# Kernel tuning notes

Hardware: AMD Instinct MI355X
Metric: run time of the kernel (lower is better)

## Reference

```python
import jax, jax.numpy as jnp
import numpy as np

N_HEAD = 16
HEAD_DIM = 128  # n_embd // n_head
EPS = 1e-6
ROPE_BASE = 10000.0


def rmsnorm(x, w):
    rms = jnp.mean(x * x, axis=-1, keepdims=True)
    return w * (x * jax.lax.rsqrt(rms + EPS))


def rope_cache(T, head_dim):
    half = head_dim // 2
    inv_freq = 1.0 / (ROPE_BASE ** (jnp.arange(half, dtype=jnp.float32) / half))
    pos = jnp.arange(T, dtype=jnp.float32)
    freqs = pos[:, None] * inv_freq[None, :]  # [T, half]
    return jnp.cos(freqs), jnp.sin(freqs)


def apply_rope(x, cos, sin):
    # x: [B, H, T, D]; cos/sin: [T, D/2]
    half = x.shape[-1] // 2
    x1, x2 = x[..., :half], x[..., half:]
    return jnp.concatenate([x1 * cos - x2 * sin, x1 * sin + x2 * cos], axis=-1)


def setup_inputs() -> dict:
    key = jax.random.key(0)
    ks = jax.random.split(key, 8)
    B, T, C, Hid = 2, 2048, 2048, 5632
    s = 0.02
    return {
        "x": jax.random.normal(ks[0], (B, T, C), dtype=jnp.float32),
        "w_norm1": jnp.ones((C,), dtype=jnp.float32),
        "w_qkv": jax.random.normal(ks[1], (C, 3 * C), dtype=jnp.float32) * s,
        "w_proj": jax.random.normal(ks[2], (C, C), dtype=jnp.float32) * s,
        "w_norm2": jnp.ones((C,), dtype=jnp.float32),
        "w1": jax.random.normal(ks[3], (C, Hid), dtype=jnp.float32) * s,
        "w2": jax.random.normal(ks[4], (C, Hid), dtype=jnp.float32) * s,
        "w3": jax.random.normal(ks[5], (Hid, C), dtype=jnp.float32) * s,
    }


def reference(x, w_norm1, w_qkv, w_proj, w_norm2, w1, w2, w3):
    B, T, C = x.shape
    H, D = N_HEAD, HEAD_DIM

    # ---- attention branch ----
    h = rmsnorm(x, w_norm1)
    qkv = h @ w_qkv  # [B, T, 3C]
    q, k, v = jnp.split(qkv, 3, axis=-1)
    q = q.reshape(B, T, H, D).transpose(0, 2, 1, 3)  # [B,H,T,D]
    k = k.reshape(B, T, H, D).transpose(0, 2, 1, 3)
    v = v.reshape(B, T, H, D).transpose(0, 2, 1, 3)

    cos, sin = rope_cache(T, D)
    q = apply_rope(q, cos, sin)
    k = apply_rope(k, cos, sin)

    att = jnp.einsum('bhqd,bhkd->bhqk', q, k) / np.sqrt(D).astype(np.float32)
    causal = jnp.tril(jnp.ones((T, T), dtype=bool))
    att = jnp.where(causal, att, -jnp.inf)
    att = jax.nn.softmax(att, axis=-1)
    out = jnp.einsum('bhqk,bhkd->bhqd', att, v)
    out = out.transpose(0, 2, 1, 3).reshape(B, T, C)
    x = x + out @ w_proj

    # ---- SwiGLU MLP branch ----
    h2 = rmsnorm(x, w_norm2)
    x = x + (jax.nn.silu(h2 @ w1) * (h2 @ w2)) @ w3
    return x
```

## Files before the change

### kernel.cpp

```cpp
#include <hip/hip_runtime.h>

typedef short s16x8 __attribute__((ext_vector_type(8)));
typedef unsigned short u16;
typedef u16 u16x8 __attribute__((ext_vector_type(8)));
typedef u16 u16x4 __attribute__((ext_vector_type(4)));
typedef float f32x4 __attribute__((ext_vector_type(4)));

#define DEVINL __device__ __forceinline__

DEVINL u16 f2bf(float f) {
    unsigned u = __float_as_uint(f);
    u += 0x7FFFu + ((u >> 16) & 1u);
    return (u16)(u >> 16);
}
DEVINL float bf2f(u16 h) { return __uint_as_float((unsigned)h << 16); }

DEVINL void gl2lds16(const void* g, void* l) {
    __builtin_amdgcn_global_load_lds((const __attribute__((address_space(1))) void*)g,
                                     (__attribute__((address_space(3))) void*)l, 16, 0, 0);
}

DEVINL void tcast_tile(const float* __restrict__ src, u16* __restrict__ dst,
                       const int K, const int N, const int kx, const int ny,
                       const int tid, float (*tile)[33])
{
    const long k0 = (long)kx * 32;
    const long n0 = (long)ny * 32;
    const int r = tid >> 3, c4 = (tid & 7) * 4;
    float4 v = *(const float4*)&src[(k0 + r) * N + n0 + c4];
    tile[r][c4] = v.x; tile[r][c4 + 1] = v.y; tile[r][c4 + 2] = v.z; tile[r][c4 + 3] = v.w;
    __syncthreads();
    u16x4 ov;
    ov[0] = f2bf(tile[c4][r]);     ov[1] = f2bf(tile[c4 + 1][r]);
    ov[2] = f2bf(tile[c4 + 2][r]); ov[3] = f2bf(tile[c4 + 3][r]);
    *(u16x4*)&dst[(n0 + r) * K + k0 + c4] = ov;
}

__global__ __launch_bounds__(256) void tcast4(
    const float* __restrict__ s0, const float* __restrict__ s1,
    const float* __restrict__ s2, const float* __restrict__ s3,
    u16* __restrict__ d0, u16* __restrict__ d1,
    u16* __restrict__ d2, u16* __restrict__ d3)
{
    __shared__ float tile[32][33];
    int t = blockIdx.x;
    const float* src; u16* dst; int N;
    if (t < 12288)      {             src = s0; dst = d0; N = 6144; }
    else if (t < 16384) { t -= 12288; src = s1; dst = d1; N = 2048; }
    else if (t < 27648) { t -= 16384; src = s2; dst = d2; N = 5632; }
    else                { t -= 27648; src = s3; dst = d3; N = 5632; }
    tcast_tile(src, dst, 2048, N, t & 63, t >> 6, threadIdx.x, tile);
}

__global__ __launch_bounds__(256) void tcast(
    const float* __restrict__ src, u16* __restrict__ dst, const int K, const int N)
{
    __shared__ float tile[32][33];
    tcast_tile(src, dst, K, N, blockIdx.x, blockIdx.y, threadIdx.x, tile);
}

__global__ __launch_bounds__(256) void rmsnorm_cast(
    const float* __restrict__ x, const float* __restrict__ wn, u16* __restrict__ out)
{
    const int C = 2048;
    const long row = blockIdx.x;
    const int tid = threadIdx.x;
    const float4* xr = (const float4*)(x + row * C);
    float4 a = xr[tid * 2], b = xr[tid * 2 + 1];
    float ss = a.x*a.x + a.y*a.y + a.z*a.z + a.w*a.w
             + b.x*b.x + b.y*b.y + b.z*b.z + b.w*b.w;
#pragma unroll
    for (int m = 1; m < 64; m <<= 1) ss += __shfl_xor(ss, m);
    __shared__ float red[4];
    if ((tid & 63) == 0) red[tid >> 6] = ss;
    __syncthreads();
    float scale = rsqrtf((red[0] + red[1] + red[2] + red[3]) * (1.f / 2048.f) + 1e-6f);
    const float4* wr = (const float4*)wn;
    float4 wa = wr[tid * 2], wb = wr[tid * 2 + 1];
    u16x8 o;
    o[0] = f2bf(a.x * scale * wa.x); o[1] = f2bf(a.y * scale * wa.y);
    o[2] = f2bf(a.z * scale * wa.z); o[3] = f2bf(a.w * scale * wa.w);
    o[4] = f2bf(b.x * scale * wb.x); o[5] = f2bf(b.y * scale * wb.y);
    o[6] = f2bf(b.z * scale * wb.z); o[7] = f2bf(b.w * scale * wb.w);
    *(u16x8*)&out[row * C + tid * 8] = o;
}

template <int MODE>
__global__ __launch_bounds__(256, 2) void gemm128(
    const u16* __restrict__ A, const u16* __restrict__ Bt,
    const int N, const int K,
    float* __restrict__ outF, u16* __restrict__ outB,
    const float* __restrict__ resid)
{
    __shared__ u16 As[128 * 64];
    __shared__ u16 Bs[128 * 64];
    const int tid = threadIdx.x;
    const int lane = tid & 63;
    const int w = tid >> 6;
    const int wm = w >> 1, wn = w & 1;
    const int quad = lane >> 4, l16 = lane & 15;
    const long m0 = (long)blockIdx.x * 128;
    const long n0 = (long)blockIdx.y * 128;

    const u16* ga[4]; const u16* gb[4]; char* la[4]; char* lb[4];
#pragma unroll
    for (int rr = 0; rr < 4; ++rr) {
        int idx = rr * 256 + tid;
        int r = idx >> 3, j = idx & 7;
        int c = (j ^ (r & 7)) * 8;
        ga[rr] = A + (m0 + r) * K + c;
        gb[rr] = Bt + (n0 + r) * K + c;
        la[rr] = (char*)As + idx * 16;
        lb[rr] = (char*)Bs + idx * 16;
    }

    f32x4 acc[4][4] = {};

    for (int k0 = 0; k0 < K; k0 += 64) {
#pragma unroll
        for (int rr = 0; rr < 4; ++rr) {
            gl2lds16(ga[rr] + k0, la[rr]);
            gl2lds16(gb[rr] + k0, lb[rr]);
        }
        __syncthreads();
#pragma unroll
        for (int ks = 0; ks < 2; ++ks) {
            s16x8 af[4], bfv[4];
#pragma unroll
            for (int mt = 0; mt < 4; ++mt)
                af[mt] = *(const s16x8*)&As[(wm * 64 + mt * 16 + l16) * 64 +
                                            ((ks * 4 + quad) ^ (l16 & 7)) * 8];
#pragma unroll
            for (int nt = 0; nt < 4; ++nt)
                bfv[nt] = *(const s16x8*)&Bs[(wn * 64 + nt * 16 + l16) * 64 +
                                             ((ks * 4 + quad) ^ (l16 & 7)) * 8];
#pragma unroll
            for (int mt = 0; mt < 4; ++mt)
#pragma unroll
                for (int nt = 0; nt < 4; ++nt)
                    acc[mt][nt] = __builtin_amdgcn_mfma_f32_16x16x32_bf16(af[mt], bfv[nt], acc[mt][nt], 0, 0, 0);
        }
        __syncthreads();
    }

#pragma unroll
    for (int mt = 0; mt < 4; ++mt)
#pragma unroll
        for (int reg = 0; reg < 4; ++reg) {
            long row = m0 + wm * 64 + mt * 16 + quad * 4 + reg;
#pragma unroll
            for (int nt = 0; nt < 4; ++nt) {
                long col = n0 + wn * 64 + nt * 16 + l16;
                float v = acc[mt][nt][reg];
                if (MODE == 0) {
                    outB[row * N + col] = f2bf(v);
                } else {
                    outF[row * N + col] = resid[row * N + col] + v;
                }
            }
        }
}

__global__ __launch_bounds__(256, 2) void gemm_ffn(
    const u16* __restrict__ A, const u16* __restrict__ B1t, const u16* __restrict__ B2t,
    const int N, const int K, u16* __restrict__ outB)
{
    __shared__ u16 As[128 * 64];
    __shared__ u16 B1s[128 * 64];
    __shared__ u16 B2s[128 * 64];
    const int tid = threadIdx.x;
    const int lane = tid & 63;
    const int w = tid >> 6;
    const int wm = w >> 1, wn = w & 1;
    const int quad = lane >> 4, l16 = lane & 15;
    const long m0 = (long)blockIdx.x * 128;
    const long n0 = (long)blockIdx.y * 128;

    const u16* ga[4]; const u16* gb1[4]; const u16* gb2[4];
    char* la[4]; char* lb1[4]; char* lb2[4];
#pragma unroll
    for (int rr = 0; rr < 4; ++rr) {
        int idx = rr * 256 + tid;
        int r = idx >> 3, j = idx & 7;
        int c = (j ^ (r & 7)) * 8;
        ga[rr]  = A + (m0 + r) * K + c;
        gb1[rr] = B1t + (n0 + r) * K + c;
        gb2[rr] = B2t + (n0 + r) * K + c;
        la[rr]  = (char*)As + idx * 16;
        lb1[rr] = (char*)B1s + idx * 16;
        lb2[rr] = (char*)B2s + idx * 16;
    }

    f32x4 acc1[4][4] = {};
    f32x4 acc2[4][4] = {};

    for (int k0 = 0; k0 < K; k0 += 64) {
#pragma unroll
        for (int rr = 0; rr < 4; ++rr) {
            gl2lds16(ga[rr] + k0, la[rr]);
            gl2lds16(gb1[rr] + k0, lb1[rr]);
            gl2lds16(gb2[rr] + k0, lb2[rr]);
        }
        __syncthreads();
#pragma unroll
        for (int ks = 0; ks < 2; ++ks) {
            s16x8 af[4], b1f[4], b2f[4];
#pragma unroll
            for (int mt = 0; mt < 4; ++mt)
                af[mt] = *(const s16x8*)&As[(wm * 64 + mt * 16 + l16) * 64 +
                                            ((ks * 4 + quad) ^ (l16 & 7)) * 8];
#pragma unroll
            for (int nt = 0; nt < 4; ++nt) {
                b1f[nt] = *(const s16x8*)&B1s[(wn * 64 + nt * 16 + l16) * 64 +
                                              ((ks * 4 + quad) ^ (l16 & 7)) * 8];
                b2f[nt] = *(const s16x8*)&B2s[(wn * 64 + nt * 16 + l16) * 64 +
                                              ((ks * 4 + quad) ^ (l16 & 7)) * 8];
            }
#pragma unroll
            for (int mt = 0; mt < 4; ++mt)
#pragma unroll
                for (int nt = 0; nt < 4; ++nt) {
                    acc1[mt][nt] = __builtin_amdgcn_mfma_f32_16x16x32_bf16(af[mt], b1f[nt], acc1[mt][nt], 0, 0, 0);
                    acc2[mt][nt] = __builtin_amdgcn_mfma_f32_16x16x32_bf16(af[mt], b2f[nt], acc2[mt][nt], 0, 0, 0);
                }
        }
        __syncthreads();
    }

#pragma unroll
    for (int mt = 0; mt < 4; ++mt)
#pragma unroll
        for (int reg = 0; reg < 4; ++reg) {
            long row = m0 + wm * 64 + mt * 16 + quad * 4 + reg;
#pragma unroll
            for (int nt = 0; nt < 4; ++nt) {
                long col = n0 + wn * 64 + nt * 16 + l16;
                float g = acc1[mt][nt][reg];
                float s = g / (1.f + __expf(-g));
                outB[row * N + col] = f2bf(s * acc2[mt][nt][reg]);
            }
        }
}

__global__ __launch_bounds__(256) void rope_qk(
    const u16* __restrict__ qkv, u16* __restrict__ qT, u16* __restrict__ kT)
{
    const int row = blockIdx.x;
    const int t = row & 2047, b = row >> 11;
    const int tid = threadIdx.x;
    __shared__ u16 buf[4096];
    const u16* src = qkv + (long)row * 6144;
    u16x8 aa = *(const u16x8*)&src[tid * 8];
    u16x8 kk = *(const u16x8*)&src[2048 + tid * 8];
    *(u16x8*)&buf[tid * 8] = aa;
    *(u16x8*)&buf[2048 + tid * 8] = kk;
    __syncthreads();
    const int c = tid * 8;
    const int h = c >> 7, dh = c & 127;
    const bool first = dh < 64;
    const int pc = first ? (c + 64) : (c - 64);
    float cs[8], sn[8];
#pragma unroll
    for (int j = 0; j < 8; ++j) {
        float inv = __expf(-(float)((dh & 63) + j) * 0.14391156831212787f);
        float ang = (float)t * inv;
        cs[j] = __cosf(ang); sn[j] = __sinf(ang);
    }
    const long obase = ((long)(b * 16 + h) * 2048 + t) * 128 + dh;
#pragma unroll
    for (int part = 0; part < 2; ++part) {
        const int base = part * 2048;
        u16x8 mine = *(const u16x8*)&buf[base + c];
        u16x8 oth  = *(const u16x8*)&buf[base + pc];
        const float qs = part ? 1.f : 0.08838834764831845f;
        u16x8 o;
#pragma unroll
        for (int j = 0; j < 8; ++j) {
            float xv = bf2f(mine[j]), yv = bf2f(oth[j]);
            float ov = first ? (xv * cs[j] - yv * sn[j]) : (yv * sn[j] + xv * cs[j]);
            o[j] = f2bf(ov * qs);
        }
        u16* dst = part ? kT : qT;
        *(u16x8*)&dst[obase] = o;
    }
}

__global__ __launch_bounds__(256) void vtrans(
    const u16* __restrict__ qkv, u16* __restrict__ vT)
{
    const int bh = blockIdx.x;
    const int b = bh >> 4, h = bh & 15;
    const int t0 = blockIdx.y * 64, d0 = blockIdx.z * 64;
    __shared__ u16 tile[64 * 65];
    const int tid = threadIdx.x;
#pragma unroll
    for (int rr = 0; rr < 2; ++rr) {
        int idx = rr * 256 + tid;
        int r = idx >> 3, c = (idx & 7) * 8;
        u16x8 v = *(const u16x8*)&qkv[(long)(b * 2048 + t0 + r) * 6144 + 4096 + h * 128 + d0 + c];
#pragma unroll
        for (int j = 0; j < 8; ++j) tile[r * 65 + c + j] = v[j];
    }
    __syncthreads();
#pragma unroll
    for (int rr = 0; rr < 2; ++rr) {
        int idx = rr * 256 + tid;
        int dd = idx >> 3, cc = (idx & 7) * 8;
        u16x8 o;
#pragma unroll
        for (int j = 0; j < 8; ++j) o[j] = tile[(cc + j) * 65 + dd];
        *(u16x8*)&vT[((long)bh * 128 + d0 + dd) * 2048 + t0 + cc] = o;
    }
}

__global__ __launch_bounds__(256, 2) void attn_kernel(
    const u16* __restrict__ qT, const u16* __restrict__ kT,
    const u16* __restrict__ vT, u16* __restrict__ outT)
{
    const int T = 2048, D = 128;
    const int lid = blockIdx.x;
    const int swz = (lid & 7) * 128 + (lid >> 3);
    const int bh = swz >> 5;
    const int qt = 31 - (swz & 31);
    const int tid = threadIdx.x, lane = tid & 63, w = tid >> 6;
    const int quad = lane >> 4, l16 = lane & 15;
    const int qrow = qt * 64 + w * 16;

    __shared__ u16 Ks[2][64 * 128];
    __shared__ u16 Vs[2][128 * 64];
    __shared__ u16 Ps[4][16 * 64];

    s16x8 aq[4];
    const u16* qb = qT + ((long)bh * T + qrow + l16) * D;
#pragma unroll
    for (int kk = 0; kk < 4; ++kk)
        aq[kk] = *(const s16x8*)&qb[kk * 32 + quad * 8];

    f32x4 o[8] = {};
    float mi[4] = {-INFINITY, -INFINITY, -INFINITY, -INFINITY};
    float li[4] = {0.f, 0.f, 0.f, 0.f};

    const u16* kg0 = kT + (long)bh * T * D;
    const u16* vg0 = vT + (long)bh * D * T;

    auto stage = [&](int kt, int b) {
        const int k0 = kt * 64;
#pragma unroll
        for (int rr = 0; rr < 4; ++rr) {
            int idx = rr * 256 + tid;
            int kr = idx >> 4, kj = idx & 15;
            gl2lds16(kg0 + (long)(k0 + kr) * D + ((kj ^ (kr & 15)) * 8),
                     (char*)Ks[b] + idx * 16);
            int vr = idx >> 3, vj = idx & 7;
            gl2lds16(vg0 + (long)vr * T + k0 + ((vj ^ (vr & 7)) * 8),
                     (char*)Vs[b] + idx * 16);
        }
    };

    stage(0, 0);

    for (int kt = 0; kt <= qt; ++kt) {
        __syncthreads();
        if (kt < qt) stage(kt + 1, (kt + 1) & 1);
        const u16* ks_ = Ks[kt & 1];
        const u16* vs_ = Vs[kt & 1];
        const int k0 = kt * 64;

        f32x4 sf[4] = {};
        __builtin_amdgcn_s_setprio(1);
#pragma unroll
        for (int kk = 0; kk < 4; ++kk) {
#pragma unroll
            for (int nt = 0; nt < 4; ++nt) {
                s16x8 kb = *(const s16x8*)&ks_[(nt * 16 + l16) * 128 +
                                               ((kk * 4 + quad) ^ (l16 & 15)) * 8];
                sf[nt] = __builtin_amdgcn_mfma_f32_16x16x32_bf16(aq[kk], kb, sf[nt], 0, 0, 0);
            }
        }
        __builtin_amdgcn_s_setprio(0);

        float S[4][4];
        if (kt == qt) {
#pragma unroll
            for (int nt = 0; nt < 4; ++nt) {
                int col = k0 + nt * 16 + l16;
#pragma unroll
                for (int reg = 0; reg < 4; ++reg) {
                    int row = qrow + quad * 4 + reg;
                    S[nt][reg] = (col <= row) ? sf[nt][reg] : -INFINITY;
                }
            }
        } else {
#pragma unroll
            for (int nt = 0; nt < 4; ++nt)
#pragma unroll
                for (int reg = 0; reg < 4; ++reg)
                    S[nt][reg] = sf[nt][reg];
        }

        float rm[4];
#pragma unroll
        for (int reg = 0; reg < 4; ++reg)
            rm[reg] = fmaxf(fmaxf(S[0][reg], S[1][reg]), fmaxf(S[2][reg], S[3][reg]));
#pragma unroll
        for (int m = 1; m < 16; m <<= 1)
#pragma unroll
            for (int reg = 0; reg < 4; ++reg)
                rm[reg] = fmaxf(rm[reg], __shfl_xor(rm[reg], m));

        int cond = 1;
#pragma unroll
        for (int reg = 0; reg < 4; ++reg)
            cond &= (rm[reg] - mi[reg] <= 8.f) ? 1 : 0;
        if (!__all(cond)) {
            float alpha[4];
#pragma unroll
            for (int reg = 0; reg < 4; ++reg) {
                float mn = fmaxf(mi[reg], rm[reg]);
                alpha[reg] = __expf(mi[reg] - mn);
                mi[reg] = mn;
                li[reg] *= alpha[reg];
            }
#pragma unroll
            for (int dt = 0; dt < 8; ++dt)
#pragma unroll
                for (int reg = 0; reg < 4; ++reg)
                    o[dt][reg] *= alpha[reg];
        }

        float rs[4] = {};
#pragma unroll
        for (int nt = 0; nt < 4; ++nt)
#pragma unroll
            for (int reg = 0; reg < 4; ++reg) {
                float p = __expf(S[nt][reg] - mi[reg]);
                S[nt][reg] = p;
                rs[reg] += p;
            }
#pragma unroll
        for (int m = 1; m < 16; m <<= 1)
#pragma unroll
            for (int reg = 0; reg < 4; ++reg)
                rs[reg] += __shfl_xor(rs[reg], m);
#pragma unroll
        for (int reg = 0; reg < 4; ++reg)
            li[reg] += rs[reg];

#pragma unroll
        for (int nt = 0; nt < 4; ++nt)
#pragma unroll
            for (int reg = 0; reg < 4; ++reg) {
                int prow = quad * 4 + reg;
                int pcol = nt * 16 + l16;
                Ps[w][prow * 64 + (((pcol >> 3) ^ (prow & 7)) * 8) + (pcol & 7)]
                    = f2bf(S[nt][reg]);
            }

        __builtin_amdgcn_s_setprio(1);
#pragma unroll
        for (int ks = 0; ks < 2; ++ks) {
            s16x8 pa = *(const s16x8*)&Ps[w][l16 * 64 +
                                             ((ks * 4 + quad) ^ (l16 & 7)) * 8];
#pragma unroll
            for (int dt = 0; dt < 8; ++dt) {
                s16x8 vb = *(const s16x8*)&vs_[(dt * 16 + l16) * 64 +
                                               ((ks * 4 + quad) ^ (l16 & 7)) * 8];
                o[dt] = __builtin_amdgcn_mfma_f32_16x16x32_bf16(pa, vb, o[dt], 0, 0, 0);
            }
        }
        __builtin_amdgcn_s_setprio(0);
    }

    const int b = bh >> 4, h = bh & 15;
#pragma unroll
    for (int reg = 0; reg < 4; ++reg) {
        float inv = 1.f / li[reg];
        int t = qrow + quad * 4 + reg;
        u16* orow = outT + ((long)(b * T + t)) * 2048 + h * 128;
#pragma unroll
        for (int dt = 0; dt < 8; ++dt)
            orow[dt * 16 + l16] = f2bf(o[dt][reg] * inv);
    }
}

extern "C" void kernel_launch(void* const* d_in, const int* in_sizes, int n_in,
                              void* d_out, int out_size, void* d_ws, size_t ws_size,
                              hipStream_t stream) {
    const float* x      = (const float*)d_in[0];
    const float* wn1    = (const float*)d_in[1];
    const float* w_qkv  = (const float*)d_in[2];
    const float* w_proj = (const float*)d_in[3];
    const float* wn2    = (const float*)d_in[4];
    const float* w1     = (const float*)d_in[5];
    const float* w2     = (const float*)d_in[6];
    const float* w3     = (const float*)d_in[7];
    float* out = (float*)d_out;

    char* p = (char*)d_ws;
    u16* Z       = (u16*)p; p += (size_t)6144 * 2048 * 2;
    u16* wproj_t = (u16*)p; p += (size_t)2048 * 2048 * 2;
    u16* w1_t    = (u16*)p; p += (size_t)5632 * 2048 * 2;
    u16* w2_t    = (u16*)p; p += (size_t)5632 * 2048 * 2;
    u16* C       = (u16*)p; p += (size_t)4096 * 2048 * 2;
    u16* D       = (u16*)p; p += (size_t)4096 * 6144 * 2;
    u16* E       = (u16*)p; p += (size_t)3 * 32 * 2048 * 128 * 2;

    u16* wqkv_t = Z;
    u16* w3_t   = Z;
    u16* qT = E;
    u16* kT = E + (size_t)32 * 2048 * 128;
    u16* vT = E + (size_t)2 * 32 * 2048 * 128;
    float* x2 = (float*)E;
    u16* uu = D;

    tcast4<<<38912, 256, 0, stream>>>(w_qkv, w_proj, w1, w2,
                                      wqkv_t, wproj_t, w1_t, w2_t);

    rmsnorm_cast<<<4096, 256, 0, stream>>>(x, wn1, C);
    gemm128<0><<<dim3(32, 48), 256, 0, stream>>>(C, wqkv_t, 6144, 2048,
                                                 nullptr, D, nullptr);
    rope_qk<<<4096, 256, 0, stream>>>(D, qT, kT);
    vtrans<<<dim3(32, 32, 2), 256, 0, stream>>>(D, vT);

    tcast<<<dim3(176, 64), 256, 0, stream>>>(w3, w3_t, 5632, 2048);

    attn_kernel<<<1024, 256, 0, stream>>>(qT, kT, vT, C);

    gemm128<1><<<dim3(32, 16), 256, 0, stream>>>(C, wproj_t, 2048, 2048,
                                                 x2, nullptr, x);
    rmsnorm_cast<<<4096, 256, 0, stream>>>(x2, wn2, C);
    gemm_ffn<<<dim3(32, 44), 256, 0, stream>>>(C, w1_t, w2_t, 5632, 2048, uu);
    gemm128<1><<<dim3(32, 16), 256, 0, stream>>>(uu, w3_t, 2048, 5632,
                                                 out, nullptr, x2);
}
```

Baseline: 837.7 us.

## Merge prep kernels into combined launches and widen GEMM K-tile to 128

Folds the first RMSNorm into the weight transpose-cast kernel. It also merges RoPE, the V transpose and the w3 transpose-cast into one launch, so independent small kernels share a grid and launch overhead drops. The generic GEMM now stages a 128-wide K slice per iteration with a 16-chunk XOR swizzle, which halves the number of barriers per output tile. In exchange, each block uses twice the LDS, which may limit how many blocks fit per CU.

```diff
diff --git a/kernel.cpp b/kernel.cpp
--- a/kernel.cpp
+++ b/kernel.cpp
@@ -36,42 +36,17 @@
     *(u16x4*)&dst[(n0 + r) * K + k0 + c4] = ov;
 }
 
-__global__ __launch_bounds__(256) void tcast4(
-    const float* __restrict__ s0, const float* __restrict__ s1,
-    const float* __restrict__ s2, const float* __restrict__ s3,
-    u16* __restrict__ d0, u16* __restrict__ d1,
-    u16* __restrict__ d2, u16* __restrict__ d3)
-{
-    __shared__ float tile[32][33];
-    int t = blockIdx.x;
-    const float* src; u16* dst; int N;
-    if (t < 12288)      {             src = s0; dst = d0; N = 6144; }
-    else if (t < 16384) { t -= 12288; src = s1; dst = d1; N = 2048; }
-    else if (t < 27648) { t -= 16384; src = s2; dst = d2; N = 5632; }
-    else                { t -= 27648; src = s3; dst = d3; N = 5632; }
-    tcast_tile(src, dst, 2048, N, t & 63, t >> 6, threadIdx.x, tile);
-}
-
-__global__ __launch_bounds__(256) void tcast(
-    const float* __restrict__ src, u16* __restrict__ dst, const int K, const int N)
-{
-    __shared__ float tile[32][33];
-    tcast_tile(src, dst, K, N, blockIdx.x, blockIdx.y, threadIdx.x, tile);
-}
-
-__global__ __launch_bounds__(256) void rmsnorm_cast(
-    const float* __restrict__ x, const float* __restrict__ wn, u16* __restrict__ out)
+DEVINL void rmsnorm_row(const float* __restrict__ x, const float* __restrict__ wn,
+                        u16* __restrict__ out, const long row, const int tid,
+                        float* red)
 {
     const int C = 2048;
-    const long row = blockIdx.x;
-    const int tid = threadIdx.x;
     const float4* xr = (const float4*)(x + row * C);
     float4 a = xr[tid * 2], b = xr[tid * 2 + 1];
     float ss = a.x*a.x + a.y*a.y + a.z*a.z + a.w*a.w
              + b.x*b.x + b.y*b.y + b.z*b.z + b.w*b.w;
 #pragma unroll
     for (int m = 1; m < 64; m <<= 1) ss += __shfl_xor(ss, m);
-    __shared__ float red[4];
     if ((tid & 63) == 0) red[tid >> 6] = ss;
     __syncthreads();
     float scale = rsqrtf((red[0] + red[1] + red[2] + red[3]) * (1.f / 2048.f) + 1e-6f);
@@ -85,15 +60,44 @@
     *(u16x8*)&out[row * C + tid * 8] = o;
 }
 
+__global__ __launch_bounds__(256) void rmsnorm_cast(
+    const float* __restrict__ x, const float* __restrict__ wn, u16* __restrict__ out)
+{
+    __shared__ float red[4];
+    rmsnorm_row(x, wn, out, blockIdx.x, threadIdx.x, red);
+}
+
+__global__ __launch_bounds__(256) void prep0(
+    const float* __restrict__ x, const float* __restrict__ wn1, u16* __restrict__ h,
+    const float* __restrict__ s0, const float* __restrict__ s1,
+    const float* __restrict__ s2, const float* __restrict__ s3,
+    u16* __restrict__ d0, u16* __restrict__ d1,
+    u16* __restrict__ d2, u16* __restrict__ d3)
+{
+    __shared__ float tile[32][33];
+    int t = blockIdx.x;
+    if (t < 4096) {
+        rmsnorm_row(x, wn1, h, t, threadIdx.x, &tile[0][0]);
+        return;
+    }
+    t -= 4096;
+    const float* src; u16* dst; int N;
+    if (t < 12288)      {             src = s0; dst = d0; N = 6144; }
+    else if (t < 16384) { t -= 12288; src = s1; dst = d1; N = 2048; }
+    else if (t < 27648) { t -= 16384; src = s2; dst = d2; N = 5632; }
+    else                { t -= 27648; src = s3; dst = d3; N = 5632; }
+    tcast_tile(src, dst, 2048, N, t & 63, t >> 6, threadIdx.x, tile);
+}
+
 template <int MODE>
-__global__ __launch_bounds__(256, 2) void gemm128(
+__global__ __launch_bounds__(256, 2) void gemm128k(
     const u16* __restrict__ A, const u16* __restrict__ Bt,
     const int N, const int K,
     float* __restrict__ outF, u16* __restrict__ outB,
     const float* __restrict__ resid)
 {
-    __shared__ u16 As[128 * 64];
-    __shared__ u16 Bs[128 * 64];
+    __shared__ u16 As[128 * 128];
+    __shared__ u16 Bs[128 * 128];
     const int tid = threadIdx.x;
     const int lane = tid & 63;
     const int w = tid >> 6;
@@ -102,38 +106,34 @@
     const long m0 = (long)blockIdx.x * 128;
     const long n0 = (long)blockIdx.y * 128;
 
-    const u16* ga[4]; const u16* gb[4]; char* la[4]; char* lb[4];
-#pragma unroll
-    for (int rr = 0; rr < 4; ++rr) {
-        int idx = rr * 256 + tid;
-        int r = idx >> 3, j = idx & 7;
-        int c = (j ^ (r & 7)) * 8;
-        ga[rr] = A + (m0 + r) * K + c;
-        gb[rr] = Bt + (n0 + r) * K + c;
-        la[rr] = (char*)As + idx * 16;
-        lb[rr] = (char*)Bs + idx * 16;
-    }
+    const int r0 = tid >> 4;
+    const int c0 = ((tid & 15) ^ r0) * 8;
+    const u16* gA = A + (m0 + r0) * K + c0;
+    const u16* gB = Bt + (n0 + r0) * K + c0;
+    char* lA = (char*)As + tid * 16;
+    char* lB = (char*)Bs + tid * 16;
+    const long rstep = (long)16 * K;
 
     f32x4 acc[4][4] = {};
 
-    for (int k0 = 0; k0 < K; k0 += 64) {
-#pragma unroll
-        for (int rr = 0; rr < 4; ++rr) {
-            gl2lds16(ga[rr] + k0, la[rr]);
-            gl2lds16(gb[rr] + k0, lb[rr]);
-        }
-        __syncthreads();
-#pragma unroll
-        for (int ks = 0; ks < 2; ++ks) {
+    for (int k0 = 0; k0 < K; k0 += 128) {
+#pragma unroll
+        for (int rr = 0; rr < 8; ++rr) {
+            gl2lds16(gA + k0 + rr * rstep, lA + rr * 4096);
+            gl2lds16(gB + k0 + rr * rstep, lB + rr * 4096);
+        }
+        __syncthreads();
+#pragma unroll
+        for (int ks = 0; ks < 4; ++ks) {
             s16x8 af[4], bfv[4];
 #pragma unroll
             for (int mt = 0; mt < 4; ++mt)
-                af[mt] = *(const s16x8*)&As[(wm * 64 + mt * 16 + l16) * 64 +
-                                            ((ks * 4 + quad) ^ (l16 & 7)) * 8];
+                af[mt] = *(const s16x8*)&As[(wm * 64 + mt * 16 + l16) * 128 +
+                                            ((ks * 4 + quad) ^ l16) * 8];
 #pragma unroll
             for (int nt = 0; nt < 4; ++nt)
-                bfv[nt] = *(const s16x8*)&Bs[(wn * 64 + nt * 16 + l16) * 64 +
-                                             ((ks * 4 + quad) ^ (l16 & 7)) * 8];
+                bfv[nt] = *(const s16x8*)&Bs[(wn * 64 + nt * 16 + l16) * 128 +
+                                             ((ks * 4 + quad) ^ l16) * 8];
 #pragma unroll
             for (int mt = 0; mt < 4; ++mt)
 #pragma unroll
@@ -242,74 +242,79 @@
         }
 }
 
-__global__ __launch_bounds__(256) void rope_qk(
-    const u16* __restrict__ qkv, u16* __restrict__ qT, u16* __restrict__ kT)
-{
-    const int row = blockIdx.x;
-    const int t = row & 2047, b = row >> 11;
+__global__ __launch_bounds__(256) void ropev(
+    const u16* __restrict__ qkv, u16* __restrict__ qT, u16* __restrict__ kT,
+    u16* __restrict__ vT, const float* __restrict__ w3, u16* __restrict__ w3t)
+{
+    __shared__ float smf[2080];
+    const int t = blockIdx.x;
     const int tid = threadIdx.x;
-    __shared__ u16 buf[4096];
-    const u16* src = qkv + (long)row * 6144;
-    u16x8 aa = *(const u16x8*)&src[tid * 8];
-    u16x8 kk = *(const u16x8*)&src[2048 + tid * 8];
-    *(u16x8*)&buf[tid * 8] = aa;
-    *(u16x8*)&buf[2048 + tid * 8] = kk;
-    __syncthreads();
-    const int c = tid * 8;
-    const int h = c >> 7, dh = c & 127;
-    const bool first = dh < 64;
-    const int pc = first ? (c + 64) : (c - 64);
-    float cs[8], sn[8];
-#pragma unroll
-    for (int j = 0; j < 8; ++j) {
-        float inv = __expf(-(float)((dh & 63) + j) * 0.14391156831212787f);
-        float ang = (float)t * inv;
-        cs[j] = __cosf(ang); sn[j] = __sinf(ang);
-    }
-    const long obase = ((long)(b * 16 + h) * 2048 + t) * 128 + dh;
-#pragma unroll
-    for (int part = 0; part < 2; ++part) {
-        const int base = part * 2048;
-        u16x8 mine = *(const u16x8*)&buf[base + c];
-        u16x8 oth  = *(const u16x8*)&buf[base + pc];
-        const float qs = part ? 1.f : 0.08838834764831845f;
-        u16x8 o;
+
+    if (t < 4096) {
+        u16* buf = (u16*)smf;
+        const int trow = t & 2047, b = t >> 11;
+        const u16* src = qkv + (long)t * 6144;
+        u16x8 aa = *(const u16x8*)&src[tid * 8];
+        u16x8 kk = *(const u16x8*)&src[2048 + tid * 8];
+        *(u16x8*)&buf[tid * 8] = aa;
+        *(u16x8*)&buf[2048 + tid * 8] = kk;
+        __syncthreads();
+        const int c = tid * 8;
+        const int h = c >> 7, dh = c & 127;
+        const bool first = dh < 64;
+        const int pc = first ? (c + 64) : (c - 64);
+        float cs[8], sn[8];
 #pragma unroll
         for (int j = 0; j < 8; ++j) {
-            float xv = bf2f(mine[j]), yv = bf2f(oth[j]);
-            float ov = first ? (xv * cs[j] - yv * sn[j]) : (yv * sn[j] + xv * cs[j]);
-            o[j] = f2bf(ov * qs);
-        }
-        u16* dst = part ? kT : qT;
-        *(u16x8*)&dst[obase] = o;
-    }
-}
-
-__global__ __launch_bounds__(256) void vtrans(
-    const u16* __restrict__ qkv, u16* __restrict__ vT)
-{
-    const int bh = blockIdx.x;
-    const int b = bh >> 4, h = bh & 15;
-    const int t0 = blockIdx.y * 64, d0 = blockIdx.z * 64;
-    __shared__ u16 tile[64 * 65];
-    const int tid = threadIdx.x;
-#pragma unroll
-    for (int rr = 0; rr < 2; ++rr) {
-        int idx = rr * 256 + tid;
-        int r = idx >> 3, c = (idx & 7) * 8;
-        u16x8 v = *(const u16x8*)&qkv[(long)(b * 2048 + t0 + r) * 6144 + 4096 + h * 128 + d0 + c];
-#pragma unroll
-        for (int j = 0; j < 8; ++j) tile[r * 65 + c + j] = v[j];
-    }
-    __syncthreads();
-#pragma unroll
-    for (int rr = 0; rr < 2; ++rr) {
-        int idx = rr * 256 + tid;
-        int dd = idx >> 3, cc = (idx & 7) * 8;
-        u16x8 o;
-#pragma unroll
-        for (int j = 0; j < 8; ++j) o[j] = tile[(cc + j) * 65 + dd];
-        *(u16x8*)&vT[((long)bh * 128 + d0 + dd) * 2048 + t0 + cc] = o;
+            float inv = __expf(-(float)((dh & 63) + j) * 0.14391156831212787f);
+            float ang = (float)trow * inv;
+            cs[j] = __cosf(ang); sn[j] = __sinf(ang);
+        }
+        const long obase = ((long)(b * 16 + h) * 2048 + trow) * 128 + dh;
+#pragma unroll
+        for (int part = 0; part < 2; ++part) {
+            const int base = part * 2048;
+            u16x8 mine = *(const u16x8*)&buf[base + c];
+            u16x8 oth  = *(const u16x8*)&buf[base + pc];
+            const float qs = part ? 1.f : 0.08838834764831845f;
+            u16x8 o;
+#pragma unroll
+            for (int j = 0; j < 8; ++j) {
+                float xv = bf2f(mine[j]), yv = bf2f(oth[j]);
+                float ov = first ? (xv * cs[j] - yv * sn[j]) : (yv * sn[j] + xv * cs[j]);
+                o[j] = f2bf(ov * qs);
+            }
+            u16* dst = part ? kT : qT;
+            *(u16x8*)&dst[obase] = o;
+        }
+    } else if (t < 6144) {
+        u16* tile = (u16*)smf;
+        const int u = t - 4096;
+        const int bh = u & 31;
+        const int b = bh >> 4, h = bh & 15;
+        const int t0 = ((u >> 5) & 31) * 64, d0 = (u >> 10) * 64;
+#pragma unroll
+        for (int rr = 0; rr < 2; ++rr) {
+            int idx = rr * 256 + tid;
+            int r = idx >> 3, c = (idx & 7) * 8;
+            u16x8 v = *(const u16x8*)&qkv[(long)(b * 2048 + t0 + r) * 6144 + 4096 + h * 128 + d0 + c];
+#pragma unroll
+            for (int j = 0; j < 8; ++j) tile[r * 65 + c + j] = v[j];
+        }
+        __syncthreads();
+#pragma unroll
+        for (int rr = 0; rr < 2; ++rr) {
+            int idx = rr * 256 + tid;
+            int dd = idx >> 3, cc = (idx & 7) * 8;
+            u16x8 o;
+#pragma unroll
+            for (int j = 0; j < 8; ++j) o[j] = tile[(cc + j) * 65 + dd];
+            *(u16x8*)&vT[((long)bh * 128 + d0 + dd) * 2048 + t0 + cc] = o;
+        }
+    } else {
+        const int v = t - 6144;
+        const int kx = v % 176, ny = v / 176;
+        tcast_tile(w3, w3t, 5632, 2048, kx, ny, tid, (float (*)[33])smf);
     }
 }
 
@@ -513,23 +518,21 @@
     float* x2 = (float*)E;
     u16* uu = D;
 
-    tcast4<<<38912, 256, 0, stream>>>(w_qkv, w_proj, w1, w2,
-                                      wqkv_t, wproj_t, w1_t, w2_t);
-
-    rmsnorm_cast<<<4096, 256, 0, stream>>>(x, wn1, C);
-    gemm128<0><<<dim3(32, 48), 256, 0, stream>>>(C, wqkv_t, 6144, 2048,
-                                                 nullptr, D, nullptr);
-    rope_qk<<<4096, 256, 0, stream>>>(D, qT, kT);
-    vtrans<<<dim3(32, 32, 2), 256, 0, stream>>>(D, vT);
-
-    tcast<<<dim3(176, 64), 256, 0, stream>>>(w3, w3_t, 5632, 2048);
+    prep0<<<43008, 256, 0, stream>>>(x, wn1, C,
+                                     w_qkv, w_proj, w1, w2,
+                                     wqkv_t, wproj_t, w1_t, w2_t);
+
+    gemm128k<0><<<dim3(32, 48), 256, 0, stream>>>(C, wqkv_t, 6144, 2048,
+                                                  nullptr, D, nullptr);
+
+    ropev<<<17408, 256, 0, stream>>>(D, qT, kT, vT, w3, w3_t);
 
     attn_kernel<<<1024, 256, 0, stream>>>(qT, kT, vT, C);
 
-    gemm128<1><<<dim3(32, 16), 256, 0, stream>>>(C, wproj_t, 2048, 2048,
-                                                 x2, nullptr, x);
+    gemm128k<1><<<dim3(32, 16), 256, 0, stream>>>(C, wproj_t, 2048, 2048,
+                                                  x2, nullptr, x);
     rmsnorm_cast<<<4096, 256, 0, stream>>>(x2, wn2, C);
     gemm_ffn<<<dim3(32, 44), 256, 0, stream>>>(C, w1_t, w2_t, 5632, 2048, uu);
-    gemm128<1><<<dim3(32, 16), 256, 0, stream>>>(uu, w3_t, 2048, 5632,
-                                                 out, nullptr, x2);
-}
+    gemm128k<1><<<dim3(32, 16), 256, 0, stream>>>(uu, w3_t, 2048, 5632,
+                                                  out, nullptr, x2);
+}
```

After: 831.7 us. Within noise of the previous version (-0.7%).
